# Performance work log

Measured on AMD Instinct MI355X. Metric: run time of the kernel, lower is better.

Reference implementation:

```python
import jax, jax.numpy as jnp
import numpy as np

NUM_HEADS = 12

def setup_inputs() -> dict:
    key = jax.random.key(0)
    ks = jax.random.split(key, 6)
    B, N, C, T = 1, 4096, 768, 16
    return {
        "x": jax.random.normal(ks[0], (B, N, C), dtype=jnp.float32),
        "templates": jax.random.normal(ks[1], (T, 3 * C, C), dtype=jnp.float32) * 0.02,
        "coeffs": jax.random.normal(ks[2], (2, T, 1), dtype=jnp.float32),
        "qkv_bias": jnp.zeros((3 * C,), dtype=jnp.float32),
        "proj_w": jax.random.normal(ks[3], (C, C), dtype=jnp.float32) * 0.02,
        "proj_b": jnp.zeros((C,), dtype=jnp.float32),
    }

def reference(x, templates, coeffs, qkv_bias, proj_w, proj_b):
    B, N, C = x.shape
    H = NUM_HEADS
    hd = C // H
    scale = hd ** -0.5
    # template bank: each of num_cf coefficient sets builds a (3C, C) weight; average them
    num_cf = coeffs.shape[0]
    qkv_w = jnp.einsum('kt,toi->oi', coeffs[:, :, 0], templates) / num_cf  # (3C, C)
    qkv = x @ qkv_w.T + qkv_bias                                          # (B, N, 3C)
    qkv = qkv.reshape(B, N, 3, H, hd).transpose(2, 0, 3, 1, 4)            # (3, B, H, N, hd)
    q, k, v = qkv[0], qkv[1], qkv[2]
    attn = jax.nn.softmax(jnp.einsum('bhnd,bhmd->bhnm', q, k) * scale, axis=-1)
    out = jnp.einsum('bhnm,bhmd->bhnd', attn, v)                          # (B, H, N, hd)
    out = out.transpose(0, 2, 1, 3).reshape(B, N, C)
    return out @ proj_w.T + proj_b
```

## Files before the change

kernel.cpp:

```cpp
#include <hip/hip_runtime.h>
#include <stdint.h>

#define N_SEQ 4096
#define C_DIM 768
#define HEADS 12
#define HD    64
#define OI    (2304*768)

typedef __attribute__((ext_vector_type(8))) short short8;
typedef __attribute__((ext_vector_type(4))) float f32x4;
typedef __attribute__((ext_vector_type(16))) float f32x16;

__device__ __forceinline__ short f2bf(float f) {
  union { float f; unsigned u; } v; v.f = f;
  unsigned r = v.u + 0x7FFF + ((v.u >> 16) & 1);
  return (short)(r >> 16);
}
__device__ __forceinline__ short f2bf_trunc(float f) {
  union { float f; unsigned u; } v; v.f = f;
  return (short)(v.u >> 16);
}

__global__ __launch_bounds__(256) void prep_qkvw(const float* __restrict__ tmpl,
                                                 const float* __restrict__ coeffs,
                                                 short* __restrict__ w_bf) {
  __shared__ float c[16];
  if (threadIdx.x < 16)
    c[threadIdx.x] = 0.5f * (coeffs[threadIdx.x] + coeffs[16 + threadIdx.x]);
  __syncthreads();
  int idx = blockIdx.x * 256 + threadIdx.x;
  int base = idx * 4;
  if (base >= OI) return;
  float ax = 0.f, ay = 0.f, az = 0.f, aw = 0.f;
#pragma unroll
  for (int t = 0; t < 16; ++t) {
    float4 v = *(const float4*)(tmpl + (size_t)t * OI + base);
    float ct = c[t];
    ax = fmaf(ct, v.x, ax); ay = fmaf(ct, v.y, ay);
    az = fmaf(ct, v.z, az); aw = fmaf(ct, v.w, aw);
  }
  short4 o = make_short4(f2bf(ax), f2bf(ay), f2bf(az), f2bf(aw));
  *(short4*)(w_bf + base) = o;
}

__global__ __launch_bounds__(256) void cvt_bf16(const float* __restrict__ src,
                                                short* __restrict__ dst, int n4) {
  int i = blockIdx.x * 256 + threadIdx.x;
  if (i >= n4) return;
  float4 v = ((const float4*)src)[i];
  ((short4*)dst)[i] = make_short4(f2bf(v.x), f2bf(v.y), f2bf(v.z), f2bf(v.w));
}

#define GST 40
#define QSCALE 0.1803368801111204f
__global__ __launch_bounds__(256) void gemm_qkv(const short* __restrict__ A,
                                                const short* __restrict__ B,
                                                const float* __restrict__ bias,
                                                short* __restrict__ qkv_out) {
  __shared__ short As[128 * GST];
  __shared__ short Bs[128 * GST];
  int tid = threadIdx.x;
  int wave = tid >> 6, lane = tid & 63, g = lane >> 4, l15 = lane & 15;
  int wm = (wave >> 1) * 64, wn = (wave & 1) * 64;
  size_t mblk = (size_t)blockIdx.x * 128;
  size_t nblk = (size_t)blockIdx.y * 128;

  f32x4 acc[4][4];
#pragma unroll
  for (int mi = 0; mi < 4; ++mi)
#pragma unroll
    for (int ni = 0; ni < 4; ++ni)
#pragma unroll
      for (int r = 0; r < 4; ++r) acc[mi][ni][r] = 0.f;

  int row0 = tid >> 2;
  int c8   = (tid & 3) * 8;

  for (int k0 = 0; k0 < 768; k0 += 32) {
    short8 a0 = *(const short8*)(A + (mblk + row0) * 768 + k0 + c8);
    short8 a1 = *(const short8*)(A + (mblk + row0 + 64) * 768 + k0 + c8);
    short8 b0 = *(const short8*)(B + (nblk + row0) * 768 + k0 + c8);
    short8 b1 = *(const short8*)(B + (nblk + row0 + 64) * 768 + k0 + c8);
    __syncthreads();
    *(short8*)(As + row0 * GST + c8) = a0;
    *(short8*)(As + (row0 + 64) * GST + c8) = a1;
    *(short8*)(Bs + row0 * GST + c8) = b0;
    *(short8*)(Bs + (row0 + 64) * GST + c8) = b1;
    __syncthreads();
    short8 af[4], bfr[4];
#pragma unroll
    for (int mi = 0; mi < 4; ++mi)
      af[mi] = *(const short8*)(As + (wm + mi * 16 + l15) * GST + g * 8);
#pragma unroll
    for (int ni = 0; ni < 4; ++ni)
      bfr[ni] = *(const short8*)(Bs + (wn + ni * 16 + l15) * GST + g * 8);
#pragma unroll
    for (int mi = 0; mi < 4; ++mi)
#pragma unroll
      for (int ni = 0; ni < 4; ++ni)
        acc[mi][ni] = __builtin_amdgcn_mfma_f32_16x16x32_bf16(af[mi], bfr[ni], acc[mi][ni], 0, 0, 0);
  }

#pragma unroll
  for (int ni = 0; ni < 4; ++ni) {
    int col = (int)nblk + wn + ni * 16 + l15;
    int which = col / 768;
    int rem = col - which * 768;
    int h = rem >> 6, d = rem & 63;
    float bcol = bias[col];
    if (which == 2) {
      short* vbase = qkv_out + (size_t)2 * HEADS * N_SEQ * HD
                   + ((size_t)h * HD + d) * N_SEQ;
#pragma unroll
      for (int mi = 0; mi < 4; ++mi) {
        int rowb = (int)mblk + wm + mi * 16 + g * 4;
        short4 o;
        o.x = f2bf(acc[mi][ni][0] + bcol);
        o.y = f2bf(acc[mi][ni][1] + bcol);
        o.z = f2bf(acc[mi][ni][2] + bcol);
        o.w = f2bf(acc[mi][ni][3] + bcol);
        *(short4*)(vbase + rowb) = o;
      }
    } else {
      float sc = (which == 0) ? QSCALE : 1.0f;
      short* dst = qkv_out + ((size_t)which * HEADS + h) * N_SEQ * HD + d;
#pragma unroll
      for (int mi = 0; mi < 4; ++mi) {
        int rowb = (int)mblk + wm + mi * 16 + g * 4;
#pragma unroll
        for (int r = 0; r < 4; ++r)
          dst[(size_t)(rowb + r) * HD] = f2bf((acc[mi][ni][r] + bcol) * sc);
      }
    }
  }
}

__global__ __launch_bounds__(256) void gemm_proj(const short* __restrict__ A,
                                                 const short* __restrict__ B,
                                                 const float* __restrict__ bias,
                                                 float* __restrict__ C) {
  __shared__ short As[64 * GST];
  __shared__ short Bs[64 * GST];
  int tid = threadIdx.x;
  int wave = tid >> 6, lane = tid & 63, g = lane >> 4, l15 = lane & 15;
  int wm = (wave >> 1) * 32, wn = (wave & 1) * 32;
  size_t mblk = (size_t)blockIdx.x * 64;
  size_t nblk = (size_t)blockIdx.y * 64;

  f32x4 acc[2][2];
#pragma unroll
  for (int mi = 0; mi < 2; ++mi)
#pragma unroll
    for (int ni = 0; ni < 2; ++ni)
#pragma unroll
      for (int r = 0; r < 4; ++r) acc[mi][ni][r] = 0.f;

  int row0 = tid >> 2;
  int c8   = (tid & 3) * 8;

  for (int k0 = 0; k0 < 768; k0 += 32) {
    short8 a0 = *(const short8*)(A + (mblk + row0) * 768 + k0 + c8);
    short8 b0 = *(const short8*)(B + (nblk + row0) * 768 + k0 + c8);
    __syncthreads();
    *(short8*)(As + row0 * GST + c8) = a0;
    *(short8*)(Bs + row0 * GST + c8) = b0;
    __syncthreads();
    short8 af[2], bfr[2];
#pragma unroll
    for (int mi = 0; mi < 2; ++mi)
      af[mi] = *(const short8*)(As + (wm + mi * 16 + l15) * GST + g * 8);
#pragma unroll
    for (int ni = 0; ni < 2; ++ni)
      bfr[ni] = *(const short8*)(Bs + (wn + ni * 16 + l15) * GST + g * 8);
#pragma unroll
    for (int mi = 0; mi < 2; ++mi)
#pragma unroll
      for (int ni = 0; ni < 2; ++ni)
        acc[mi][ni] = __builtin_amdgcn_mfma_f32_16x16x32_bf16(af[mi], bfr[ni], acc[mi][ni], 0, 0, 0);
  }

#pragma unroll
  for (int ni = 0; ni < 2; ++ni) {
    int col = (int)nblk + wn + ni * 16 + l15;
    float bcol = bias[col];
#pragma unroll
    for (int mi = 0; mi < 2; ++mi) {
      int rowb = (int)mblk + wm + mi * 16 + g * 4;
#pragma unroll
      for (int r = 0; r < 4; ++r)
        C[(size_t)(rowb + r) * 768 + col] = acc[mi][ni][r] + bcol;
    }
  }
}

#define PST 68
__global__ __launch_bounds__(256, 2) void attn_fa(const short* __restrict__ qkv_buf,
                                                  float* __restrict__ op0,
                                                  float* __restrict__ op1,
                                                  float* __restrict__ lp) {
  __shared__ short Ks[64 * PST];
  __shared__ short Vt[64 * PST];
  __shared__ short Ps[128 * PST];
  int bid = blockIdx.x;
  int j = (bid & 7) * 96 + (bid >> 3);
  int h = j >> 6;
  int rj = j & 63;
  int half = rj >> 5;
  int qt = rj & 31;
  int tid = threadIdx.x, wave = tid >> 6, lane = tid & 63;
  int q5 = lane & 31, h5 = lane >> 5;
  int qb = qt * 128 + wave * 32;
  int kvb = half * 2048;
  const short* qh  = qkv_buf + (size_t)(0 * HEADS + h) * N_SEQ * HD;
  const short* kh  = qkv_buf + (size_t)(1 * HEADS + h) * N_SEQ * HD;
  const short* vth = qkv_buf + (size_t)2 * HEADS * N_SEQ * HD + (size_t)h * HD * N_SEQ;

  short8 qf[4];
#pragma unroll
  for (int c = 0; c < 4; ++c)
    qf[c] = *(const short8*)(qh + (size_t)(qb + q5) * HD + c * 16 + h5 * 8);

  f32x16 o_acc[2];
#pragma unroll
  for (int dt = 0; dt < 2; ++dt)
#pragma unroll
    for (int r = 0; r < 16; ++r) o_acc[dt][r] = 0.f;
  float l_r = 0.f;

  int srow = tid >> 2;
  int sq   = (tid & 3) * 16;

  short8 kr[2], vr[2];
#pragma unroll
  for (int i = 0; i < 2; ++i) {
    kr[i] = *(const short8*)(kh + (size_t)(kvb + srow) * HD + sq + 8 * i);
    vr[i] = *(const short8*)(vth + (size_t)srow * N_SEQ + kvb + sq + 8 * i);
  }

  short* pw = Ps + wave * 32 * PST;

  for (int t0 = kvb; t0 < kvb + 2048; t0 += 64) {
    __syncthreads();
#pragma unroll
    for (int i = 0; i < 2; ++i) {
      *(short8*)(Ks + srow * PST + sq + 8 * i) = kr[i];
      *(short8*)(Vt + srow * PST + sq + 8 * i) = vr[i];
    }
    __syncthreads();

    if (t0 + 64 < kvb + 2048) {
      int t1 = t0 + 64;
#pragma unroll
      for (int i = 0; i < 2; ++i) {
        kr[i] = *(const short8*)(kh + (size_t)(t1 + srow) * HD + sq + 8 * i);
        vr[i] = *(const short8*)(vth + (size_t)srow * N_SEQ + t1 + sq + 8 * i);
      }
    }

    f32x16 st[2];
#pragma unroll
    for (int kt = 0; kt < 2; ++kt)
#pragma unroll
      for (int r = 0; r < 16; ++r) st[kt][r] = 0.f;
#pragma unroll
    for (int c = 0; c < 4; ++c)
#pragma unroll
      for (int kt = 0; kt < 2; ++kt) {
        short8 kf = *(const short8*)(Ks + (kt * 32 + q5) * PST + c * 16 + h5 * 8);
        st[kt] = __builtin_amdgcn_mfma_f32_32x32x16_bf16(kf, qf[c], st[kt], 0, 0, 0);
      }

#pragma unroll
    for (int kt = 0; kt < 2; ++kt)
#pragma unroll
      for (int cc = 0; cc < 4; ++cc) {
        float p0 = __builtin_amdgcn_exp2f(st[kt][cc * 4 + 0]);
        float p1 = __builtin_amdgcn_exp2f(st[kt][cc * 4 + 1]);
        float p2 = __builtin_amdgcn_exp2f(st[kt][cc * 4 + 2]);
        float p3 = __builtin_amdgcn_exp2f(st[kt][cc * 4 + 3]);
        l_r += (p0 + p1) + (p2 + p3);
        short4 o = make_short4(f2bf_trunc(p0), f2bf_trunc(p1), f2bf_trunc(p2), f2bf_trunc(p3));
        *(short4*)(pw + q5 * PST + kt * 32 + cc * 8 + h5 * 4) = o;
      }

#pragma unroll
    for (int c = 0; c < 4; ++c) {
      short8 pf = *(const short8*)(pw + q5 * PST + c * 16 + h5 * 8);
#pragma unroll
      for (int dt = 0; dt < 2; ++dt) {
        short8 vf = *(const short8*)(Vt + (dt * 32 + q5) * PST + c * 16 + h5 * 8);
        o_acc[dt] = __builtin_amdgcn_mfma_f32_32x32x16_bf16(pf, vf, o_acc[dt], 0, 0, 0);
      }
    }
  }

  float* op = half ? op1 : op0;
  float l = l_r + __shfl_xor(l_r, 32);
#pragma unroll
  for (int cc = 0; cc < 4; ++cc)
#pragma unroll
    for (int rr = 0; rr < 4; ++rr) {
      int qloc = rr + 8 * cc + 4 * h5;
      size_t base = ((size_t)h * N_SEQ + qb + qloc) * HD;
#pragma unroll
      for (int dt = 0; dt < 2; ++dt)
        op[base + dt * 32 + q5] = o_acc[dt][cc * 4 + rr];
    }
  if (h5 == 0)
    lp[((size_t)half * HEADS + h) * N_SEQ + qb + q5] = l;
}

__global__ __launch_bounds__(256) void attn_reduce(const float* __restrict__ op0,
                                                   const float* __restrict__ op1,
                                                   const float* __restrict__ lp,
                                                   short* __restrict__ out_bf) {
  int idx = blockIdx.x * 256 + threadIdx.x;
  int d4 = idx & 15;
  int n  = (idx >> 4) & 4095;
  int h  = idx >> 16;
  size_t o = ((size_t)h * N_SEQ + n) * HD + d4 * 4;
  float4 a = *(const float4*)(op0 + o);
  float4 b = *(const float4*)(op1 + o);
  float l = lp[(size_t)h * N_SEQ + n] + lp[((size_t)HEADS + h) * N_SEQ + n];
  float inv = 1.0f / l;
  short4 s = make_short4(f2bf((a.x + b.x) * inv), f2bf((a.y + b.y) * inv),
                         f2bf((a.z + b.z) * inv), f2bf((a.w + b.w) * inv));
  *(short4*)(out_bf + (size_t)n * C_DIM + h * HD + d4 * 4) = s;
}

extern "C" void kernel_launch(void* const* d_in, const int* in_sizes, int n_in,
                              void* d_out, int out_size, void* d_ws, size_t ws_size,
                              hipStream_t stream) {
  const float* x        = (const float*)d_in[0];
  const float* tmpl     = (const float*)d_in[1];
  const float* coeffs   = (const float*)d_in[2];
  const float* qkv_bias = (const float*)d_in[3];
  const float* proj_w   = (const float*)d_in[4];
  const float* proj_b   = (const float*)d_in[5];
  float* out = (float*)d_out;
  char* ws = (char*)d_ws;

  short* w_bf    = (short*)(ws);
  short* x_bf    = (short*)(ws + 3538944);
  short* pw_bf   = (short*)(ws + 9830400);
  short* qkvb    = (short*)(ws + 11010048);
  short* attn_bf = (short*)(ws + 29884416);
  float* opart1  = (float*)(ws + 36175872);
  float* lpart   = (float*)(ws + 48758784);
  float* opart0  = out;

  prep_qkvw<<<1728, 256, 0, stream>>>(tmpl, coeffs, w_bf);
  cvt_bf16<<<3072, 256, 0, stream>>>(x, x_bf, 786432);
  cvt_bf16<<<576, 256, 0, stream>>>(proj_w, pw_bf, 147456);

  dim3 g1(32, 18);
  gemm_qkv<<<g1, 256, 0, stream>>>(x_bf, w_bf, qkv_bias, qkvb);

  attn_fa<<<768, 256, 0, stream>>>(qkvb, opart0, opart1, lpart);
  attn_reduce<<<3072, 256, 0, stream>>>(opart0, opart1, lpart, attn_bf);

  dim3 g2(64, 12);
  gemm_proj<<<g2, 256, 0, stream>>>(attn_bf, pw_bf, proj_b, out);
}
```

Before: 339.6 us.

## Keep P in registers via permlane swap and double-buffer K/V in LDS

The attention kernel no longer round-trips the softmax probabilities through shared memory. It packs them with v_cvt_pk_bf16_f32 and rearranges them across lanes with v_permlane32_swap so they can feed the PV MFMA directly as operands. K/V tiles are now double-buffered in LDS, which removes one __syncthreads per iteration and lets the next tile's store overlap compute. The change also switches P conversion from truncation to round-to-nearest and relies on gfx950-specific instructions in inline asm.

```diff
diff --git a/kernel.cpp b/kernel.cpp
--- a/kernel.cpp
+++ b/kernel.cpp
@@ -15,10 +15,6 @@
   union { float f; unsigned u; } v; v.f = f;
   unsigned r = v.u + 0x7FFF + ((v.u >> 16) & 1);
   return (short)(r >> 16);
-}
-__device__ __forceinline__ short f2bf_trunc(float f) {
-  union { float f; unsigned u; } v; v.f = f;
-  return (short)(v.u >> 16);
 }
 
 __global__ __launch_bounds__(256) void prep_qkvw(const float* __restrict__ tmpl,
@@ -198,9 +194,8 @@
                                                   float* __restrict__ op0,
                                                   float* __restrict__ op1,
                                                   float* __restrict__ lp) {
-  __shared__ short Ks[64 * PST];
-  __shared__ short Vt[64 * PST];
-  __shared__ short Ps[128 * PST];
+  __shared__ short Ks[2][64 * PST];
+  __shared__ short Vt[2][64 * PST];
   int bid = blockIdx.x;
   int j = (bid & 7) * 96 + (bid >> 3);
   int h = j >> 6;
@@ -236,26 +231,36 @@
     kr[i] = *(const short8*)(kh + (size_t)(kvb + srow) * HD + sq + 8 * i);
     vr[i] = *(const short8*)(vth + (size_t)srow * N_SEQ + kvb + sq + 8 * i);
   }
-
-  short* pw = Ps + wave * 32 * PST;
-
-  for (int t0 = kvb; t0 < kvb + 2048; t0 += 64) {
-    __syncthreads();
-#pragma unroll
-    for (int i = 0; i < 2; ++i) {
-      *(short8*)(Ks + srow * PST + sq + 8 * i) = kr[i];
-      *(short8*)(Vt + srow * PST + sq + 8 * i) = vr[i];
+#pragma unroll
+  for (int i = 0; i < 2; ++i) {
+    *(short8*)(&Ks[0][srow * PST + sq + 8 * i]) = kr[i];
+    *(short8*)(&Vt[0][srow * PST + sq + 8 * i]) = vr[i];
+  }
+#pragma unroll
+  for (int i = 0; i < 2; ++i) {
+    kr[i] = *(const short8*)(kh + (size_t)(kvb + 64 + srow) * HD + sq + 8 * i);
+    vr[i] = *(const short8*)(vth + (size_t)srow * N_SEQ + kvb + 64 + sq + 8 * i);
+  }
+
+  for (int it = 0; it < 32; ++it) {
+    int cur = it & 1;
+    __syncthreads();
+
+    if (it + 1 < 32) {
+#pragma unroll
+      for (int i = 0; i < 2; ++i) {
+        *(short8*)(&Ks[cur ^ 1][srow * PST + sq + 8 * i]) = kr[i];
+        *(short8*)(&Vt[cur ^ 1][srow * PST + sq + 8 * i]) = vr[i];
+      }
+      if (it + 2 < 32) {
+        int t2 = kvb + (it + 2) * 64;
+#pragma unroll
+        for (int i = 0; i < 2; ++i) {
+          kr[i] = *(const short8*)(kh + (size_t)(t2 + srow) * HD + sq + 8 * i);
+          vr[i] = *(const short8*)(vth + (size_t)srow * N_SEQ + t2 + sq + 8 * i);
+        }
+      }
     }
-    __syncthreads();
-
-    if (t0 + 64 < kvb + 2048) {
-      int t1 = t0 + 64;
-#pragma unroll
-      for (int i = 0; i < 2; ++i) {
-        kr[i] = *(const short8*)(kh + (size_t)(t1 + srow) * HD + sq + 8 * i);
-        vr[i] = *(const short8*)(vth + (size_t)srow * N_SEQ + t1 + sq + 8 * i);
-      }
-    }
 
     f32x16 st[2];
 #pragma unroll
@@ -266,32 +271,43 @@
     for (int c = 0; c < 4; ++c)
 #pragma unroll
       for (int kt = 0; kt < 2; ++kt) {
-        short8 kf = *(const short8*)(Ks + (kt * 32 + q5) * PST + c * 16 + h5 * 8);
+        short8 kf = *(const short8*)(&Ks[cur][(kt * 32 + q5) * PST + c * 16 + h5 * 8]);
         st[kt] = __builtin_amdgcn_mfma_f32_32x32x16_bf16(kf, qf[c], st[kt], 0, 0, 0);
       }
 
+    short8 pf[4];
 #pragma unroll
     for (int kt = 0; kt < 2; ++kt)
 #pragma unroll
-      for (int cc = 0; cc < 4; ++cc) {
-        float p0 = __builtin_amdgcn_exp2f(st[kt][cc * 4 + 0]);
-        float p1 = __builtin_amdgcn_exp2f(st[kt][cc * 4 + 1]);
-        float p2 = __builtin_amdgcn_exp2f(st[kt][cc * 4 + 2]);
-        float p3 = __builtin_amdgcn_exp2f(st[kt][cc * 4 + 3]);
-        l_r += (p0 + p1) + (p2 + p3);
-        short4 o = make_short4(f2bf_trunc(p0), f2bf_trunc(p1), f2bf_trunc(p2), f2bf_trunc(p3));
-        *(short4*)(pw + q5 * PST + kt * 32 + cc * 8 + h5 * 4) = o;
-      }
-
-#pragma unroll
-    for (int c = 0; c < 4; ++c) {
-      short8 pf = *(const short8*)(pw + q5 * PST + c * 16 + h5 * 8);
+      for (int cm = 0; cm < 2; ++cm) {
+        float p0 = __builtin_amdgcn_exp2f(st[kt][cm * 8 + 0]);
+        float p1 = __builtin_amdgcn_exp2f(st[kt][cm * 8 + 1]);
+        float p2 = __builtin_amdgcn_exp2f(st[kt][cm * 8 + 2]);
+        float p3 = __builtin_amdgcn_exp2f(st[kt][cm * 8 + 3]);
+        float p4 = __builtin_amdgcn_exp2f(st[kt][cm * 8 + 4]);
+        float p5 = __builtin_amdgcn_exp2f(st[kt][cm * 8 + 5]);
+        float p6 = __builtin_amdgcn_exp2f(st[kt][cm * 8 + 6]);
+        float p7 = __builtin_amdgcn_exp2f(st[kt][cm * 8 + 7]);
+        l_r += ((p0 + p1) + (p2 + p3)) + ((p4 + p5) + (p6 + p7));
+        unsigned X1, Y1, X2, Y2;
+        asm("v_cvt_pk_bf16_f32 %0, %1, %2" : "=v"(X1) : "v"(p0), "v"(p1));
+        asm("v_cvt_pk_bf16_f32 %0, %1, %2" : "=v"(Y1) : "v"(p4), "v"(p5));
+        asm("v_cvt_pk_bf16_f32 %0, %1, %2" : "=v"(X2) : "v"(p2), "v"(p3));
+        asm("v_cvt_pk_bf16_f32 %0, %1, %2" : "=v"(Y2) : "v"(p6), "v"(p7));
+        asm("v_permlane32_swap_b32 %0, %1" : "+v"(X1), "+v"(Y1));
+        asm("v_permlane32_swap_b32 %0, %1" : "+v"(X2), "+v"(Y2));
+        union { unsigned u[4]; short8 s; } w;
+        w.u[0] = X1; w.u[1] = X2; w.u[2] = Y1; w.u[3] = Y2;
+        pf[kt * 2 + cm] = w.s;
+      }
+
+#pragma unroll
+    for (int c = 0; c < 4; ++c)
 #pragma unroll
       for (int dt = 0; dt < 2; ++dt) {
-        short8 vf = *(const short8*)(Vt + (dt * 32 + q5) * PST + c * 16 + h5 * 8);
-        o_acc[dt] = __builtin_amdgcn_mfma_f32_32x32x16_bf16(pf, vf, o_acc[dt], 0, 0, 0);
-      }
-    }
+        short8 vf = *(const short8*)(&Vt[cur][(dt * 32 + q5) * PST + c * 16 + h5 * 8]);
+        o_acc[dt] = __builtin_amdgcn_mfma_f32_32x32x16_bf16(pf[c], vf, o_acc[dt], 0, 0, 0);
+      }
   }
 
   float* op = half ? op1 : op0;
```

Result: faster. 306.2 us (-9.9%).
